# Optimization experiments

Hardware: AMD Instinct MI355X
Metric: run time of the kernel (lower is better)

## Reference

```python
import jax, jax.numpy as jnp
import numpy as np
import math

N_EMBD = 512
N_BRANCH = 4
BLOCK = 2048
B, T = 2, 2048


def make_rope_tables(dim, max_len):
    inv_freq = 1.0 / (10000.0 ** (np.arange(0, dim, 2, dtype=np.float32) / dim))
    t = np.arange(max_len, dtype=np.float32)
    freqs = np.einsum('i,j->ij', t, inv_freq)  # [max_len, dim/2]
    return jnp.asarray(np.cos(freqs)), jnp.asarray(np.sin(freqs))


def apply_rope(xq, cos, sin):
    # xq: [..., T, C]; cos/sin: [T, C/2]
    x1 = xq[..., 0::2]
    x2 = xq[..., 1::2]
    y1 = x1 * cos - x2 * sin
    y2 = x1 * sin + x2 * cos
    return jnp.stack((y1, y2), axis=-1).reshape(xq.shape)


def setup_inputs() -> dict:
    key = jax.random.key(0)
    ks = jax.random.split(key, 6)
    C, NB = N_EMBD, N_BRANCH
    s = 1.0 / math.sqrt(C)
    a = jax.random.normal(ks[0], (B, T, C), jnp.float32)
    x = jax.random.normal(ks[1], (B, T, C), jnp.float32)
    Wq = jax.random.normal(ks[2], (C, C * NB), jnp.float32) * s
    Wk = jax.random.normal(ks[3], (C, C), jnp.float32) * s
    Wv = jax.random.normal(ks[4], (C, C * NB), jnp.float32) * s
    Wo = jax.random.normal(ks[5], (C, C), jnp.float32) * s
    cos, sin = make_rope_tables(C, BLOCK)
    return {"a": a, "x": x, "Wq": Wq, "Wk": Wk, "Wv": Wv, "Wo": Wo,
            "cos": cos, "sin": sin}


def reference(a, x, Wq, Wk, Wv, Wo, cos, sin):
    Bb, Tt, C = x.shape
    NB = Wq.shape[1] // C
    cos_t = cos[:Tt]
    sin_t = sin[:Tt]

    q = (a @ Wq).reshape(Bb, Tt, NB, C).transpose(0, 2, 1, 3)  # [B,NB,T,C]
    v = (a @ Wv).reshape(Bb, Tt, NB, C).transpose(0, 2, 1, 3)  # [B,NB,T,C]
    k = (x @ Wk)[:, None, :, :]                                # [B,1,T,C]

    q = apply_rope(q, cos_t, sin_t)
    k = apply_rope(k, cos_t, sin_t)

    att = jnp.einsum('bntc,bosc->bnts', q, k) / math.sqrt(C)   # [B,NB,T,T]
    causal = jnp.tril(jnp.ones((Tt, Tt), bool))                # [T,T]
    att_m = jnp.where(causal, att, -jnp.inf)

    # softmax over branch axis; mask is identical across branches, so compute
    # on unmasked logits and zero-out masked positions (== nan_to_num of
    # softmax over fully -inf columns)
    soft_probs = jnp.where(causal, jax.nn.softmax(att, axis=1), 0.0)

    max_val = jnp.max(soft_probs, axis=1, keepdims=True)
    hard_mask = jax.lax.stop_gradient((soft_probs == max_val).astype(att.dtype))
    route_mask = jax.lax.stop_gradient(hard_mask - soft_probs) + soft_probs

    att_max = jnp.max(att_m, axis=1)                           # [B,T,T]
    attn_probs = jax.nn.softmax(att_max, axis=-1)              # [B,T,T]

    combined = attn_probs[:, None, :, :] * route_mask          # [B,NB,T,T]
    y = jnp.einsum('bnts,bnsc->btc', combined, v)              # [B,T,C]
    return y @ Wo
```

## Files before the change

kernel.cpp:

```cpp
#include <hip/hip_runtime.h>
#include <math.h>


#define B_ 2
#define T_ 2048
#define C_ 512
#define NB_ 4
#define C2_ 1024

typedef unsigned short u16;
typedef unsigned char u8;
using short8 = __attribute__((ext_vector_type(8))) short;
using bf16x8 = __attribute__((ext_vector_type(8))) __bf16;
using f32x4  = __attribute__((ext_vector_type(4))) float;

__device__ __forceinline__ float bf2f(u16 u) {
  union { unsigned int i; float f; } v; v.i = ((unsigned int)u) << 16; return v.f;
}
__device__ __forceinline__ u16 f2bf(float f) {
  union { float f; unsigned int i; } v; v.f = f;
  unsigned int u = v.i;
  return (u16)((u + 0x7fffu + ((u >> 16) & 1u)) >> 16);
}
__device__ __forceinline__ f32x4 mfma16x16x32(short8 a, short8 b, f32x4 c) {
  return __builtin_amdgcn_mfma_f32_16x16x32_bf16(
      __builtin_bit_cast(bf16x8, a), __builtin_bit_cast(bf16x8, b), c, 0, 0, 0);
}
__device__ __forceinline__ void split8(const float* s, uint4& hi, uint4& lo) {
  u16 h[8], l[8];
#pragma unroll
  for (int j = 0; j < 8; ++j) {
    h[j] = f2bf(s[j]);
    l[j] = f2bf(s[j] - bf2f(h[j]));
  }
  hi.x = h[0] | ((unsigned)h[1] << 16); hi.y = h[2] | ((unsigned)h[3] << 16);
  hi.z = h[4] | ((unsigned)h[5] << 16); hi.w = h[6] | ((unsigned)h[7] << 16);
  lo.x = l[0] | ((unsigned)l[1] << 16); lo.y = l[2] | ((unsigned)l[3] << 16);
  lo.z = l[4] | ((unsigned)l[5] << 16); lo.w = l[6] | ((unsigned)l[7] << 16);
}
__device__ __forceinline__ int swz(int row) { return ((row >> 1) & 3) << 3; }

template <int MODE>
__global__ __launch_bounds__(256) void gemm_qk(const float* __restrict__ A,
                                               const float* __restrict__ W,
                                               u16* __restrict__ out,
                                               const float* __restrict__ cosT,
                                               const float* __restrict__ sinT,
                                               const int N, const int K) {
  __shared__ u16 Ah[64][32], Al[64][32];
  __shared__ u16 Bh[64][32], Bl[64][32];
  const int tid = threadIdx.x;
  const int wave = tid >> 6, lane = tid & 63;
  const int m0 = blockIdx.y << 6, n0 = blockIdx.x << 6;
  const f32x4 zero = {0.f, 0.f, 0.f, 0.f};
  f32x4 acc[4] = {zero, zero, zero, zero};
  const int srow = tid >> 2, koff = ((tid & 3) << 3) ^ swz(tid >> 2);
  const int lrow = lane & 15, lk = ((lane >> 4) << 3) ^ swz(lane & 15);
  for (int kk = 0; kk < K; kk += 32) {
    const int kg = (tid & 3) << 3;
    float av[8];
    *(float4*)(av) = *(const float4*)(&A[(size_t)(m0 + srow) * K + kk + kg]);
    *(float4*)(av + 4) =
        *(const float4*)(&A[(size_t)(m0 + srow) * K + kk + kg + 4]);
    uint4 hi, lo;
    split8(av, hi, lo);
    *(uint4*)(&Ah[srow][koff]) = hi;
    *(uint4*)(&Al[srow][koff]) = lo;
    float wv[8];
#pragma unroll
    for (int j = 0; j < 8; ++j)
      wv[j] = W[(size_t)(kk + kg + j) * N + n0 + srow];
    split8(wv, hi, lo);
    *(uint4*)(&Bh[srow][koff]) = hi;
    *(uint4*)(&Bl[srow][koff]) = lo;
    __syncthreads();
    short8 ah = *(const short8*)(&Ah[(wave << 4) + lrow][lk]);
    short8 al = *(const short8*)(&Al[(wave << 4) + lrow][lk]);
#pragma unroll
    for (int ns = 0; ns < 4; ++ns) {
      short8 bh = *(const short8*)(&Bh[(ns << 4) + lrow][lk]);
      short8 bl = *(const short8*)(&Bl[(ns << 4) + lrow][lk]);
      acc[ns] = mfma16x16x32(ah, bh, acc[ns]);
      acc[ns] = mfma16x16x32(al, bh, acc[ns]);
      acc[ns] = mfma16x16x32(ah, bl, acc[ns]);
    }
    __syncthreads();
  }
  const int r0 = m0 + (wave << 4) + ((lane >> 4) << 2);
  const int cb = n0 + (lane & 15);
#pragma unroll
  for (int ns = 0; ns < 4; ++ns) {
#pragma unroll
    for (int r = 0; r < 4; ++r) {
      const int rg = r0 + r;
      const int cg = cb + (ns << 4);
      float v = acc[ns][r];
      float pv = __shfl_xor(v, 1);
      const int t = rg & (T_ - 1);
      const int c = (MODE == 1) ? (cg & (C_ - 1)) : cg;
      const int i = c >> 1;
      const float cf = cosT[(t << 8) + i];
      const float sf = sinT[(t << 8) + i];
      float x1 = (lane & 1) ? pv : v;
      float x2 = (lane & 1) ? v : pv;
      float y = (lane & 1) ? (x1 * sf + x2 * cf) : (x1 * cf - x2 * sf);
      if (MODE == 1) y *= 0.044194173824159216f;
      const u16 hi = f2bf(y);
      const u16 lo = f2bf(y - bf2f(hi));
      size_t rowoff;
      if (MODE == 1) {
        const int b = rg >> 11, n = cg >> 9;
        rowoff = ((size_t)((b * NB_ + n) * T_ + t)) * C2_;
      } else {
        rowoff = (size_t)rg * C2_;
      }
      out[rowoff + c] = hi;
      out[rowoff + C_ + c] = lo;
    }
  }
}

template <int AF32, int OF32>
__global__ __launch_bounds__(256) void gemm_hi(const void* __restrict__ Ap,
                                               const float* __restrict__ W,
                                               void* __restrict__ outp,
                                               const int N, const int K) {
  __shared__ u16 As[64][32];
  __shared__ u16 Bs[64][32];
  const int tid = threadIdx.x;
  const int wave = tid >> 6, lane = tid & 63;
  const int m0 = blockIdx.y << 6, n0 = blockIdx.x << 6;
  const f32x4 zero = {0.f, 0.f, 0.f, 0.f};
  f32x4 acc[4] = {zero, zero, zero, zero};
  const int srow = tid >> 2, koff = ((tid & 3) << 3) ^ swz(tid >> 2);
  const int lrow = lane & 15, lk = ((lane >> 4) << 3) ^ swz(lane & 15);
  for (int kk = 0; kk < K; kk += 32) {
    const int kg = (tid & 3) << 3;
    if (AF32) {
      const float* A = (const float*)Ap;
      float av[8];
      *(float4*)(av) = *(const float4*)(&A[(size_t)(m0 + srow) * K + kk + kg]);
      *(float4*)(av + 4) =
          *(const float4*)(&A[(size_t)(m0 + srow) * K + kk + kg + 4]);
      uint4 hi;
      hi.x = f2bf(av[0]) | ((unsigned)f2bf(av[1]) << 16);
      hi.y = f2bf(av[2]) | ((unsigned)f2bf(av[3]) << 16);
      hi.z = f2bf(av[4]) | ((unsigned)f2bf(av[5]) << 16);
      hi.w = f2bf(av[6]) | ((unsigned)f2bf(av[7]) << 16);
      *(uint4*)(&As[srow][koff]) = hi;
    } else {
      const u16* A = (const u16*)Ap;
      *(uint4*)(&As[srow][koff]) =
          *(const uint4*)(&A[(size_t)(m0 + srow) * K + kk + kg]);
    }
    uint4 hi;
    {
      float w[8];
#pragma unroll
      for (int j = 0; j < 8; ++j)
        w[j] = W[(size_t)(kk + kg + j) * N + n0 + srow];
      hi.x = f2bf(w[0]) | ((unsigned)f2bf(w[1]) << 16);
      hi.y = f2bf(w[2]) | ((unsigned)f2bf(w[3]) << 16);
      hi.z = f2bf(w[4]) | ((unsigned)f2bf(w[5]) << 16);
      hi.w = f2bf(w[6]) | ((unsigned)f2bf(w[7]) << 16);
    }
    *(uint4*)(&Bs[srow][koff]) = hi;
    __syncthreads();
    short8 af = *(const short8*)(&As[(wave << 4) + lrow][lk]);
#pragma unroll
    for (int ns = 0; ns < 4; ++ns) {
      short8 bf = *(const short8*)(&Bs[(ns << 4) + lrow][lk]);
      acc[ns] = mfma16x16x32(af, bf, acc[ns]);
    }
    __syncthreads();
  }
  const int r0 = m0 + (wave << 4) + ((lane >> 4) << 2);
  const int cb = n0 + (lane & 15);
#pragma unroll
  for (int ns = 0; ns < 4; ++ns) {
#pragma unroll
    for (int r = 0; r < 4; ++r) {
      const size_t idx = (size_t)(r0 + r) * N + cb + (ns << 4);
      if (OF32) ((float*)outp)[idx] = acc[ns][r];
      else ((u16*)outp)[idx] = f2bf(acc[ns][r]);
    }
  }
}

__global__ __launch_bounds__(256) void transpose_v_k(const u16* __restrict__ Vraw,
                                                     u16* __restrict__ VT) {
  const int bid = blockIdx.x;
  const int ct = bid & 7;
  const int ttile = (bid >> 3) & 31;
  const int n = (bid >> 8) & 3;
  const int b = bid >> 10;
  __shared__ u16 tile[64][68];
  const int tid = threadIdx.x;
  const int rr = tid >> 4;
  const int cc = (tid & 15) << 2;
  const int t0 = ttile << 6, c0 = ct << 6;
#pragma unroll
  for (int it = 0; it < 4; ++it) {
    const int r = (it << 4) + rr;
    *(ushort4*)(&tile[r][cc]) = *(const ushort4*)(
        &Vraw[((size_t)((b << 11) + t0 + r)) * (NB_ * C_) + n * C_ + c0 + cc]);
  }
  __syncthreads();
#pragma unroll
  for (int it = 0; it < 4; ++it) {
    const int c = (it << 4) + rr;
    ushort4 w;
    w.x = tile[cc + 0][c]; w.y = tile[cc + 1][c];
    w.z = tile[cc + 2][c]; w.w = tile[cc + 3][c];
    *(ushort4*)(&VT[((size_t)((b * NB_ + n) * C_ + c0 + c)) * T_ + t0 + cc]) = w;
  }
}

__global__ __launch_bounds__(256) void scores_k(const u16* __restrict__ Qcat,
                                                const u16* __restrict__ Kcat,
                                                u16* __restrict__ Mout,
                                                u8* __restrict__ Mask) {
  const int tri = ((blockIdx.x & 7) * 66) + (blockIdx.x >> 3);
  int tt = (int)((sqrtf(8.f * (float)tri + 1.f) - 1.f) * 0.5f);
  while ((tt + 1) * (tt + 2) / 2 <= tri) ++tt;
  while (tt * (tt + 1) / 2 > tri) --tt;
  const int ss = tri - tt * (tt + 1) / 2;
  const int b = blockIdx.y;
  __shared__ u16 Qh[NB_][64][32], Ql[NB_][64][32];
  __shared__ u16 Kh[64][32], Kl[64][32];
  const int tid = threadIdx.x;
  const int wave = tid >> 6, lane = tid & 63;
  const int t0 = tt << 6, s0 = ss << 6;
  const f32x4 zero = {0.f, 0.f, 0.f, 0.f};
  f32x4 acc[NB_][4];
  for (int n = 0; n < NB_; ++n)
    for (int j = 0; j < 4; ++j) acc[n][j] = zero;
  const int srow = tid >> 2, koff = ((tid & 3) << 3) ^ swz(tid >> 2);
  const int lrow = lane & 15, lk = ((lane >> 4) << 3) ^ swz(lane & 15);
  const int kg = (tid & 3) << 3;
  for (int kk = 0; kk < C_; kk += 32) {
#pragma unroll
    for (int n = 0; n < NB_; ++n) {
      const size_t qb =
          ((size_t)((b * NB_ + n) * T_ + t0 + srow)) * C2_ + kk + kg;
      *(uint4*)(&Qh[n][srow][koff]) = *(const uint4*)(&Qcat[qb]);
      *(uint4*)(&Ql[n][srow][koff]) = *(const uint4*)(&Qcat[qb + C_]);
    }
    const size_t kb = ((size_t)((b << 11) + s0 + srow)) * C2_ + kk + kg;
    *(uint4*)(&Kh[srow][koff]) = *(const uint4*)(&Kcat[kb]);
    *(uint4*)(&Kl[srow][koff]) = *(const uint4*)(&Kcat[kb + C_]);
    __syncthreads();
    short8 qh[NB_], ql[NB_];
#pragma unroll
    for (int n = 0; n < NB_; ++n) {
      qh[n] = *(const short8*)(&Qh[n][(wave << 4) + lrow][lk]);
      ql[n] = *(const short8*)(&Ql[n][(wave << 4) + lrow][lk]);
    }
#pragma unroll
    for (int ns = 0; ns < 4; ++ns) {
      short8 kh = *(const short8*)(&Kh[(ns << 4) + lrow][lk]);
      short8 kl = *(const short8*)(&Kl[(ns << 4) + lrow][lk]);
#pragma unroll
      for (int n = 0; n < NB_; ++n) {
        acc[n][ns] = mfma16x16x32(qh[n], kh, acc[n][ns]);
        acc[n][ns] = mfma16x16x32(ql[n], kh, acc[n][ns]);
        acc[n][ns] = mfma16x16x32(qh[n], kl, acc[n][ns]);
      }
    }
    __syncthreads();
  }
  const int tb = t0 + (wave << 4) + ((lane >> 4) << 2);
  const int sb = s0 + (lane & 15);
#pragma unroll
  for (int ns = 0; ns < 4; ++ns) {
#pragma unroll
    for (int r = 0; r < 4; ++r) {
      const int t = tb + r, s = sb + (ns << 4);
      float a0 = acc[0][ns][r], a1 = acc[1][ns][r];
      float a2 = acc[2][ns][r], a3 = acc[3][ns][r];
      float m = fmaxf(fmaxf(a0, a1), fmaxf(a2, a3));
      u8 msk = (u8)((a0 == m) | ((a1 == m) << 1) | ((a2 == m) << 2) |
                    ((a3 == m) << 3));
      if (s > t) { m = -__builtin_inff(); msk = 0; }
      const size_t idx = (size_t)b * T_ * T_ + (size_t)t * T_ + s;
      Mout[idx] = f2bf(m);
      Mask[idx] = msk;
    }
  }
}

__global__ __launch_bounds__(256) void rowstats_k(const u16* __restrict__ Mb,
                                                  float* __restrict__ Rm,
                                                  float* __restrict__ Rz) {
  const int r = (blockIdx.x << 2) + (threadIdx.x >> 6);
  const int lane = threadIdx.x & 63;
  const int b = r >> 11, t = r & (T_ - 1);
  const u16* row = Mb + (size_t)b * T_ * T_ + (size_t)t * T_;
  float m = -__builtin_inff();
  for (int s = lane; s <= t; s += 64) m = fmaxf(m, bf2f(row[s]));
#pragma unroll
  for (int off = 32; off; off >>= 1) m = fmaxf(m, __shfl_xor(m, off));
  float z = 0.f;
  for (int s = lane; s <= t; s += 64) z += __expf(bf2f(row[s]) - m);
#pragma unroll
  for (int off = 32; off; off >>= 1) z += __shfl_xor(z, off);
  if (lane == 0) { Rm[r] = m; Rz[r] = 1.f / z; }
}

__global__ __launch_bounds__(512) void pv_k(const u16* __restrict__ Mb,
                                            const float* __restrict__ Rm,
                                            const float* __restrict__ Rz,
                                            const u8* __restrict__ Mask,
                                            const u16* __restrict__ VT,
                                            u16* __restrict__ Y) {
  const int bid = blockIdx.x, b = blockIdx.y;
  const int cblk = bid & 7;
  const int tt = 31 - (bid >> 3);
  const int c0 = cblk << 6;
  __shared__ u16 Ps[NB_][64][32];
  __shared__ u16 Vs[NB_][64][32];
  const int tid = threadIdx.x;
  const int wave = tid >> 6, lane = tid & 63;
  const int wq = wave & 3, ch = wave >> 2;
  const int row8 = tid >> 3, off4 = (tid & 7) << 2;
  const int scol = off4 ^ swz(row8);
  const int lrow = lane & 15, lk = ((lane >> 4) << 3) ^ swz(lane & 15);
  const f32x4 zero = {0.f, 0.f, 0.f, 0.f};
  const size_t vrow_base[NB_] = {
      ((size_t)((b * NB_ + 0) * C_ + c0 + row8)) * T_,
      ((size_t)((b * NB_ + 1) * C_ + c0 + row8)) * T_,
      ((size_t)((b * NB_ + 2) * C_ + c0 + row8)) * T_,
      ((size_t)((b * NB_ + 3) * C_ + c0 + row8)) * T_};

  const int t0 = tt << 6;
  const int nchunk = (tt + 1) << 1;
  const int rg = (b << 11) + t0 + row8;
  const size_t pro = (size_t)rg << 11;
  const float rm = Rm[rg], rz = Rz[rg];
  f32x4 acc[2] = {zero, zero};
  uint2 pu; unsigned mk1; uint2 vv[NB_];
  pu = *(const uint2*)(&Mb[pro + off4]);
  mk1 = *(const unsigned*)(&Mask[pro + off4]);
#pragma unroll
  for (int n = 0; n < NB_; ++n)
    vv[n] = *(const uint2*)(&VT[vrow_base[n] + off4]);
  for (int ck = 0; ck < nchunk; ++ck) {
    u16 m4[4] = {(u16)pu.x, (u16)(pu.x >> 16), (u16)pu.y, (u16)(pu.y >> 16)};
    u16 p[4];
#pragma unroll
    for (int j = 0; j < 4; ++j)
      p[j] = f2bf(__expf(bf2f(m4[j]) - rm) * rz);
    u8 mk[4] = {(u8)mk1, (u8)(mk1 >> 8), (u8)(mk1 >> 16), (u8)(mk1 >> 24)};
#pragma unroll
    for (int n = 0; n < NB_; ++n) {
      uint2 wv;
      wv.x = (unsigned)(((mk[0] >> n) & 1) ? p[0] : 0) |
             ((unsigned)(((mk[1] >> n) & 1) ? p[1] : 0) << 16);
      wv.y = (unsigned)(((mk[2] >> n) & 1) ? p[2] : 0) |
             ((unsigned)(((mk[3] >> n) & 1) ? p[3] : 0) << 16);
      *(uint2*)(&Ps[n][row8][scol]) = wv;
      *(uint2*)(&Vs[n][row8][scol]) = vv[n];
    }
    __syncthreads();
    if (ck + 1 < nchunk) {
      const int sB = (ck + 1) << 5;
      pu = *(const uint2*)(&Mb[pro + sB + off4]);
      mk1 = *(const unsigned*)(&Mask[pro + sB + off4]);
#pragma unroll
      for (int n = 0; n < NB_; ++n)
        vv[n] = *(const uint2*)(&VT[vrow_base[n] + sB + off4]);
    }
#pragma unroll
    for (int n = 0; n < NB_; ++n) {
      short8 af = *(const short8*)(&Ps[n][(wq << 4) + lrow][lk]);
#pragma unroll
      for (int cs = 0; cs < 2; ++cs) {
        short8 bf =
            *(const short8*)(&Vs[n][(ch << 5) + (cs << 4) + lrow][lk]);
        acc[cs] = mfma16x16x32(af, bf, acc[cs]);
      }
    }
    __syncthreads();
  }
  const int tb = t0 + (wq << 4) + ((lane >> 4) << 2);
  const int cbs = c0 + (ch << 5) + (lane & 15);
#pragma unroll
  for (int cs = 0; cs < 2; ++cs) {
#pragma unroll
    for (int r = 0; r < 4; ++r) {
      Y[(size_t)((b << 11) + tb + r) * C_ + cbs + (cs << 4)] =
          f2bf(acc[cs][r]);
    }
  }
}

extern "C" void kernel_launch(void* const* d_in, const int* in_sizes, int n_in,
                              void* d_out, int out_size, void* d_ws,
                              size_t ws_size, hipStream_t stream) {
  (void)in_sizes; (void)n_in; (void)out_size; (void)ws_size;
  const float* a    = (const float*)d_in[0];
  const float* x    = (const float*)d_in[1];
  const float* Wq   = (const float*)d_in[2];
  const float* Wk   = (const float*)d_in[3];
  const float* Wv   = (const float*)d_in[4];
  const float* Wo   = (const float*)d_in[5];
  const float* cosT = (const float*)d_in[6];
  const float* sinT = (const float*)d_in[7];

  char* w = (char*)d_ws;
  u16* Qcat   = (u16*)(w + 0);
  u16* Kcat   = (u16*)(w + 33554432);
  u16* Vraw   = (u16*)(w + 41943040);
  u16* VT     = (u16*)(w + 58720256);
  u8*  Mask   = (u8*)(w + 75497472);
  float* Rm   = (float*)(w + 83886080);
  float* Rz   = (float*)(w + 83902464);
  u16* Mb     = Vraw;
  u16* Y      = Qcat;

  const dim3 blk(256);
  gemm_qk<1><<<dim3(32, 64), blk, 0, stream>>>(a, Wq, Qcat, cosT, sinT, 2048, 512);
  gemm_qk<2><<<dim3(8, 64), blk, 0, stream>>>(x, Wk, Kcat, cosT, sinT, 512, 512);
  gemm_hi<1, 0><<<dim3(32, 64), blk, 0, stream>>>(a, Wv, (void*)Vraw, 2048, 512);
  transpose_v_k<<<dim3(2048), blk, 0, stream>>>(Vraw, VT);
  scores_k<<<dim3(528, 2), blk, 0, stream>>>(Qcat, Kcat, Mb, Mask);
  rowstats_k<<<dim3(1024), blk, 0, stream>>>(Mb, Rm, Rz);
  pv_k<<<dim3(256, 2), dim3(512), 0, stream>>>(Mb, Rm, Rz, Mask, VT, Y);
  gemm_hi<0, 1><<<dim3(8, 64), blk, 0, stream>>>(Y, Wo, d_out, 512, 512);
}
```

Baseline: 379.3 us.

## Balance causal PV work by pairing short and long 32-row tiles per block

The PV kernel moves to 256-thread blocks that each process two 32-row query tiles: one from the start and one from the end of the causal triangle. Every block then does roughly equal work, avoiding tail imbalance from long diagonal blocks. V tiles are loaded with wider 16-byte loads but reused across only 32 rows instead of 64, which increases V traffic.

```diff
diff --git a/kernel.cpp b/kernel.cpp
--- a/kernel.cpp
+++ b/kernel.cpp
@@ -307,7 +307,7 @@
   if (lane == 0) { Rm[r] = m; Rz[r] = 1.f / z; }
 }
 
-__global__ __launch_bounds__(512) void pv_k(const u16* __restrict__ Mb,
+__global__ __launch_bounds__(256) void pv_k(const u16* __restrict__ Mb,
                                             const float* __restrict__ Rm,
                                             const float* __restrict__ Rz,
                                             const u8* __restrict__ Mask,
@@ -315,81 +315,87 @@
                                             u16* __restrict__ Y) {
   const int bid = blockIdx.x, b = blockIdx.y;
   const int cblk = bid & 7;
-  const int tt = 31 - (bid >> 3);
+  const int y = bid >> 3;
   const int c0 = cblk << 6;
-  __shared__ u16 Ps[NB_][64][32];
+  __shared__ u16 Ps[NB_][32][32];
   __shared__ u16 Vs[NB_][64][32];
   const int tid = threadIdx.x;
   const int wave = tid >> 6, lane = tid & 63;
-  const int wq = wave & 3, ch = wave >> 2;
-  const int row8 = tid >> 3, off4 = (tid & 7) << 2;
-  const int scol = off4 ^ swz(row8);
+  const int wq = wave & 1, ch = wave >> 1;
+  const int prow = tid >> 3, poff = (tid & 7) << 2;
+  const int pcol = poff ^ swz(prow);
+  const int vrow = tid >> 2, voff = (tid & 3) << 3;
+  const int vcol = voff ^ swz(vrow);
   const int lrow = lane & 15, lk = ((lane >> 4) << 3) ^ swz(lane & 15);
   const f32x4 zero = {0.f, 0.f, 0.f, 0.f};
   const size_t vrow_base[NB_] = {
-      ((size_t)((b * NB_ + 0) * C_ + c0 + row8)) * T_,
-      ((size_t)((b * NB_ + 1) * C_ + c0 + row8)) * T_,
-      ((size_t)((b * NB_ + 2) * C_ + c0 + row8)) * T_,
-      ((size_t)((b * NB_ + 3) * C_ + c0 + row8)) * T_};
-
-  const int t0 = tt << 6;
-  const int nchunk = (tt + 1) << 1;
-  const int rg = (b << 11) + t0 + row8;
-  const size_t pro = (size_t)rg << 11;
-  const float rm = Rm[rg], rz = Rz[rg];
-  f32x4 acc[2] = {zero, zero};
-  uint2 pu; unsigned mk1; uint2 vv[NB_];
-  pu = *(const uint2*)(&Mb[pro + off4]);
-  mk1 = *(const unsigned*)(&Mask[pro + off4]);
-#pragma unroll
-  for (int n = 0; n < NB_; ++n)
-    vv[n] = *(const uint2*)(&VT[vrow_base[n] + off4]);
-  for (int ck = 0; ck < nchunk; ++ck) {
-    u16 m4[4] = {(u16)pu.x, (u16)(pu.x >> 16), (u16)pu.y, (u16)(pu.y >> 16)};
-    u16 p[4];
-#pragma unroll
-    for (int j = 0; j < 4; ++j)
-      p[j] = f2bf(__expf(bf2f(m4[j]) - rm) * rz);
-    u8 mk[4] = {(u8)mk1, (u8)(mk1 >> 8), (u8)(mk1 >> 16), (u8)(mk1 >> 24)};
-#pragma unroll
-    for (int n = 0; n < NB_; ++n) {
-      uint2 wv;
-      wv.x = (unsigned)(((mk[0] >> n) & 1) ? p[0] : 0) |
-             ((unsigned)(((mk[1] >> n) & 1) ? p[1] : 0) << 16);
-      wv.y = (unsigned)(((mk[2] >> n) & 1) ? p[2] : 0) |
-             ((unsigned)(((mk[3] >> n) & 1) ? p[3] : 0) << 16);
-      *(uint2*)(&Ps[n][row8][scol]) = wv;
-      *(uint2*)(&Vs[n][row8][scol]) = vv[n];
-    }
-    __syncthreads();
-    if (ck + 1 < nchunk) {
-      const int sB = (ck + 1) << 5;
-      pu = *(const uint2*)(&Mb[pro + sB + off4]);
-      mk1 = *(const unsigned*)(&Mask[pro + sB + off4]);
-#pragma unroll
-      for (int n = 0; n < NB_; ++n)
-        vv[n] = *(const uint2*)(&VT[vrow_base[n] + sB + off4]);
-    }
-#pragma unroll
-    for (int n = 0; n < NB_; ++n) {
-      short8 af = *(const short8*)(&Ps[n][(wq << 4) + lrow][lk]);
-#pragma unroll
-      for (int cs = 0; cs < 2; ++cs) {
-        short8 bf =
-            *(const short8*)(&Vs[n][(ch << 5) + (cs << 4) + lrow][lk]);
-        acc[cs] = mfma16x16x32(af, bf, acc[cs]);
-      }
-    }
-    __syncthreads();
-  }
-  const int tb = t0 + (wq << 4) + ((lane >> 4) << 2);
-  const int cbs = c0 + (ch << 5) + (lane & 15);
-#pragma unroll
-  for (int cs = 0; cs < 2; ++cs) {
-#pragma unroll
-    for (int r = 0; r < 4; ++r) {
-      Y[(size_t)((b << 11) + tb + r) * C_ + cbs + (cs << 4)] =
-          f2bf(acc[cs][r]);
+      ((size_t)((b * NB_ + 0) * C_ + c0 + vrow)) * T_,
+      ((size_t)((b * NB_ + 1) * C_ + c0 + vrow)) * T_,
+      ((size_t)((b * NB_ + 2) * C_ + c0 + vrow)) * T_,
+      ((size_t)((b * NB_ + 3) * C_ + c0 + vrow)) * T_};
+
+  for (int h = 0; h < 2; ++h) {
+    const int tt = h ? (31 - y) : y;
+    const int z = h;
+    const int t0 = (tt << 6) + (z << 5);
+    const int nchunk = (tt << 1) + z + 1;
+    const int rg = (b << 11) + t0 + prow;
+    const size_t pro = (size_t)rg << 11;
+    const float rm = Rm[rg], rz = Rz[rg];
+    f32x4 acc[2] = {zero, zero};
+    uint2 pu; unsigned mk1; uint4 vv[NB_];
+    pu = *(const uint2*)(&Mb[pro + poff]);
+    mk1 = *(const unsigned*)(&Mask[pro + poff]);
+#pragma unroll
+    for (int n = 0; n < NB_; ++n)
+      vv[n] = *(const uint4*)(&VT[vrow_base[n] + voff]);
+    for (int ck = 0; ck < nchunk; ++ck) {
+      u16 m4[4] = {(u16)pu.x, (u16)(pu.x >> 16), (u16)pu.y, (u16)(pu.y >> 16)};
+      u16 p[4];
+#pragma unroll
+      for (int j = 0; j < 4; ++j)
+        p[j] = f2bf(__expf(bf2f(m4[j]) - rm) * rz);
+      u8 mk[4] = {(u8)mk1, (u8)(mk1 >> 8), (u8)(mk1 >> 16), (u8)(mk1 >> 24)};
+#pragma unroll
+      for (int n = 0; n < NB_; ++n) {
+        uint2 wv;
+        wv.x = (unsigned)(((mk[0] >> n) & 1) ? p[0] : 0) |
+               ((unsigned)(((mk[1] >> n) & 1) ? p[1] : 0) << 16);
+        wv.y = (unsigned)(((mk[2] >> n) & 1) ? p[2] : 0) |
+               ((unsigned)(((mk[3] >> n) & 1) ? p[3] : 0) << 16);
+        *(uint2*)(&Ps[n][prow][pcol]) = wv;
+        *(uint4*)(&Vs[n][vrow][vcol]) = vv[n];
+      }
+      __syncthreads();
+      if (ck + 1 < nchunk) {
+        const int sB = (ck + 1) << 5;
+        pu = *(const uint2*)(&Mb[pro + sB + poff]);
+        mk1 = *(const unsigned*)(&Mask[pro + sB + poff]);
+#pragma unroll
+        for (int n = 0; n < NB_; ++n)
+          vv[n] = *(const uint4*)(&VT[vrow_base[n] + sB + voff]);
+      }
+#pragma unroll
+      for (int n = 0; n < NB_; ++n) {
+        short8 af = *(const short8*)(&Ps[n][(wq << 4) + lrow][lk]);
+#pragma unroll
+        for (int cs = 0; cs < 2; ++cs) {
+          short8 bf =
+              *(const short8*)(&Vs[n][(ch << 5) + (cs << 4) + lrow][lk]);
+          acc[cs] = mfma16x16x32(af, bf, acc[cs]);
+        }
+      }
+      __syncthreads();
+    }
+    const int tb = t0 + (wq << 4) + ((lane >> 4) << 2);
+    const int cbs = c0 + (ch << 5) + (lane & 15);
+#pragma unroll
+    for (int cs = 0; cs < 2; ++cs) {
+#pragma unroll
+      for (int r = 0; r < 4; ++r) {
+        Y[(size_t)((b << 11) + tb + r) * C_ + cbs + (cs << 4)] =
+            f2bf(acc[cs][r]);
+      }
     }
   }
 }
@@ -425,6 +431,6 @@
   transpose_v_k<<<dim3(2048), blk, 0, stream>>>(Vraw, VT);
   scores_k<<<dim3(528, 2), blk, 0, stream>>>(Qcat, Kcat, Mb, Mask);
   rowstats_k<<<dim3(1024), blk, 0, stream>>>(Mb, Rm, Rz);
-  pv_k<<<dim3(256, 2), dim3(512), 0, stream>>>(Mb, Rm, Rz, Mask, VT, Y);
+  pv_k<<<dim3(256, 2), blk, 0, stream>>>(Mb, Rm, Rz, Mask, VT, Y);
   gemm_hi<0, 1><<<dim3(8, 64), blk, 0, stream>>>(Y, Wo, d_out, 512, 512);
 }
```

Measured after the change: 456.6 us. +20.4%, slower.
